# Kernel tuning notes

Measured on AMD Instinct MI355X. Metric: run time of the kernel, lower is better.

## Reference

```python
import jax, jax.numpy as jnp
import numpy as np

NUM_IMUS = 13
NUM_PARAMS = 9
EPS = 1e-5
LN_EPS = 1e-5


def setup_inputs() -> dict:
    key = jax.random.key(0)
    k1, k2, k3 = jax.random.split(key, 3)
    d_model, S = 512, 2048
    hidden_states = jax.random.normal(k1, (1, S, d_model), dtype=jnp.float32)
    min_orig_accel_norm = jax.random.normal(k2, (1,), dtype=jnp.float32)
    W = jax.random.normal(k3, (d_model, NUM_IMUS * NUM_PARAMS), dtype=jnp.float32) * 0.02
    b = jnp.zeros((NUM_IMUS * NUM_PARAMS,), jnp.float32)
    ln_w = jnp.ones((d_model,), jnp.float32)
    ln_b = jnp.zeros((d_model,), jnp.float32)
    return {"hidden_states": hidden_states, "min_orig_accel_norm": min_orig_accel_norm,
            "ln_w": ln_w, "ln_b": ln_b, "W": W, "b": b}


def _layernorm(x, w, bias):
    mu = x.mean(-1, keepdims=True)
    var = ((x - mu) ** 2).mean(-1, keepdims=True)
    return (x - mu) * jax.lax.rsqrt(var + LN_EPS) * w + bias


def reference(hidden_states, min_orig_accel_norm, ln_w, ln_b, W, b):
    S = hidden_states.shape[1]
    x = _layernorm(hidden_states, ln_w, ln_b)
    # (1,S,117) -> (S, 9, 13); batch is always 1
    p = (x @ W + b).reshape(S, NUM_PARAMS, NUM_IMUS)
    c, c_th, phi, phi_th = p[:, 4], p[:, 5], p[:, 6], p[:, 7]  # (S,13) each
    d = jnp.sqrt(p[:, 1] ** 2 + EPS)                 # (S,13)
    k = d ** 2 / 4 + jax.nn.softplus(p[:, 0])
    d_th = jnp.sqrt(p[:, 3] ** 2 + EPS)
    k_th = d_th ** 2 / 4 + jax.nn.softplus(p[:, 2])
    noise_bias = p[:, 8].T                           # (13,S)
    om = jnp.sqrt(4 * k - d ** 2) / 2                # = sqrt(softplus(p0))
    om_th = jnp.sqrt(4 * k_th - d_th ** 2) / 2
    t = jnp.arange(S, dtype=jnp.float32)
    tstep = jnp.triu(t[None, :] - t[:, None])        # (S,S), entry (i,j)=j-i for j>=i
    ts = tstep[:, :, None]                           # (S,S,1)

    def src(a):  # params indexed by source step i, broadcast over target step j
        return a[:, None, :]                         # (S,1,13)

    lin = src(c) * jnp.exp(-src(d) / 2 * ts) * jnp.sin(ts * src(om) + src(phi))
    ang = src(c_th) * jnp.exp(-src(d_th) / 2 * ts) * jnp.sin(ts * src(om_th) + src(phi_th))
    mask = jnp.triu(jnp.ones((S, S), jnp.float32))[:, :, None]
    summed = ((lin + ang) * mask).sum(axis=0)        # (S,13): sum over source i<=j
    return summed.T + min_orig_accel_norm + noise_bias  # (13,S)
```

## Files before the change

### kernel.cpp

```cpp
#include <hip/hip_runtime.h>
#include <math.h>

#define S_LEN 2048
#define D_MODEL 512
#define NIMU 13
#define NCOL 117
#define PCHUNK (S_LEN * NCOL)
#define WP_STRIDE 128

static __device__ __forceinline__ float softplus_f(float x) {
    return (x > 20.f) ? x : log1pf(expf(x));
}

__global__ __launch_bounds__(256) void stats_kernel(const float* __restrict__ H,
                                                    float2* __restrict__ stats,
                                                    const float* __restrict__ W,
                                                    float* __restrict__ Wp) {
    if (threadIdx.x < WP_STRIDE) {
        int c = threadIdx.x;
        Wp[blockIdx.x * WP_STRIDE + c] = (c < NCOL) ? W[blockIdx.x * NCOL + c] : 0.f;
    }
    int wave = threadIdx.x >> 6;
    int lane = threadIdx.x & 63;
    int row = blockIdx.x * 4 + wave;
    const float* hr = H + row * D_MODEL;
    float4 a = *(const float4*)&hr[lane * 4];
    float4 b = *(const float4*)&hr[256 + lane * 4];
    float sum = a.x + a.y + a.z + a.w + b.x + b.y + b.z + b.w;
    #pragma unroll
    for (int off = 32; off; off >>= 1) sum += __shfl_down(sum, off);
    sum = __shfl(sum, 0);
    float mu = sum * (1.f / 512.f);
    float vs = 0.f;
    vs += (a.x - mu) * (a.x - mu); vs += (a.y - mu) * (a.y - mu);
    vs += (a.z - mu) * (a.z - mu); vs += (a.w - mu) * (a.w - mu);
    vs += (b.x - mu) * (b.x - mu); vs += (b.y - mu) * (b.y - mu);
    vs += (b.z - mu) * (b.z - mu); vs += (b.w - mu) * (b.w - mu);
    #pragma unroll
    for (int off = 32; off; off >>= 1) vs += __shfl_down(vs, off);
    if (lane == 0) {
        float var = vs * (1.f / 512.f);
        stats[row] = make_float2(mu, 1.0f / sqrtf(var + 1e-5f));
    }
}

template <int ATOMIC>
__global__ __launch_bounds__(128) void proj_kernel(
    const float* __restrict__ H, const float2* __restrict__ stats,
    const float* __restrict__ lnw, const float* __restrict__ lnb,
    const float* __restrict__ Wp, float* __restrict__ Pout)
{
    __shared__ float Xt[64 * 32];
    __shared__ float Ws[64 * WP_STRIDE];
    int tid = threadIdx.x;
    int row0 = blockIdx.x * 32;
    int k0 = blockIdx.y * 64;

    {
        const float4* Wp4 = (const float4*)(Wp + k0 * WP_STRIDE);
        float4* Ws4 = (float4*)Ws;
        #pragma unroll
        for (int i = 0; i < 16; ++i) Ws4[tid + i * 128] = Wp4[tid + i * 128];
    }
    {
        int r = tid >> 2, fq = tid & 3;
        int row = row0 + r;
        float2 st = stats[row];
        const float4* H4 = (const float4*)(H + row * D_MODEL + k0);
        const float4* w4 = (const float4*)(lnw + k0);
        const float4* b4 = (const float4*)(lnb + k0);
        #pragma unroll
        for (int it = 0; it < 4; ++it) {
            int q = fq + it * 4;
            float4 h = H4[q], wv = w4[q], bv = b4[q];
            Xt[(4 * q + 0) * 32 + r] = (h.x - st.x) * st.y * wv.x + bv.x;
            Xt[(4 * q + 1) * 32 + r] = (h.y - st.x) * st.y * wv.y + bv.y;
            Xt[(4 * q + 2) * 32 + r] = (h.z - st.x) * st.y * wv.z + bv.z;
            Xt[(4 * q + 3) * 32 + r] = (h.w - st.x) * st.y * wv.w + bv.w;
        }
    }
    __syncthreads();

    int q8 = tid & 15;
    int rg = tid >> 4;
    float acc[4][8];
    #pragma unroll
    for (int a = 0; a < 4; ++a)
        for (int u = 0; u < 8; ++u) acc[a][u] = 0.f;

    #pragma unroll 4
    for (int k = 0; k < 64; ++k) {
        float4 xa = *(float4*)&Xt[k * 32 + 4 * rg];
        float4 w0 = *(float4*)&Ws[k * WP_STRIDE + 8 * q8];
        float4 w1 = *(float4*)&Ws[k * WP_STRIDE + 8 * q8 + 4];
        float xv[4] = {xa.x, xa.y, xa.z, xa.w};
        float wv[8] = {w0.x, w0.y, w0.z, w0.w, w1.x, w1.y, w1.z, w1.w};
        #pragma unroll
        for (int a = 0; a < 4; ++a)
            #pragma unroll
            for (int u = 0; u < 8; ++u)
                acc[a][u] = fmaf(xv[a], wv[u], acc[a][u]);
    }

    if (q8 < 15) {
        float* Pk = ATOMIC ? Pout : (Pout + blockIdx.y * PCHUNK);
        #pragma unroll
        for (int a = 0; a < 4; ++a) {
            int row = row0 + 4 * rg + a;
            #pragma unroll
            for (int u = 0; u < 8; ++u) {
                int c = 8 * q8 + u;
                if (c < NCOL) {
                    if (ATOMIC) atomicAdd(&Pk[row * NCOL + c], acc[a][u]);
                    else        Pk[row * NCOL + c] = acc[a][u];
                }
            }
        }
    }
}

__global__ __launch_bounds__(256) void transform_kernel(
    const float* __restrict__ Pp, int nkc,
    const float* __restrict__ bias, const float* __restrict__ minp,
    float4* __restrict__ PARL, float4* __restrict__ PARA,
    float* __restrict__ out)
{
    int t = blockIdx.x * 256 + threadIdx.x;
    if (t >= S_LEN * NIMU) return;
    int s = t / NIMU;
    int m = t - s * NIMU;
    float pv[9];
    #pragma unroll
    for (int pp = 0; pp < 9; ++pp) {
        float v = bias[pp * NIMU + m];
        for (int kc = 0; kc < nkc; ++kc)
            v += Pp[kc * PCHUNK + s * NCOL + pp * NIMU + m];
        pv[pp] = v;
    }

    const float LOG2E = 1.4426950408889634f;
    const float INV2PI = 0.15915494309189535f;
    {
        float d = sqrtf(pv[1] * pv[1] + 1e-5f);
        float kk = d * d * 0.25f + softplus_f(pv[0]);
        float om = 0.5f * sqrtf(fmaxf(4.f * kk - d * d, 0.f));
        PARL[m * S_LEN + s] = make_float4(pv[4], -0.5f * d * LOG2E, om * INV2PI, pv[6] * INV2PI);
    }
    {
        float d = sqrtf(pv[3] * pv[3] + 1e-5f);
        float kk = d * d * 0.25f + softplus_f(pv[2]);
        float om = 0.5f * sqrtf(fmaxf(4.f * kk - d * d, 0.f));
        PARA[m * S_LEN + s] = make_float4(pv[5], -0.5f * d * LOG2E, om * INV2PI, pv[7] * INV2PI);
    }
    out[m * S_LEN + s] = minp[0] + pv[8];
}

__global__ __launch_bounds__(256) void main_kernel(
    const float4* __restrict__ PARL, const float4* __restrict__ PARA,
    float* __restrict__ out)
{
    __shared__ float buf[4 * 192];
    int tid = threadIdx.x;
    int lane = tid & 63, w = tid >> 6;
    int m = blockIdx.y;
    int bx = blockIdx.x;

    int g = 0, base = 0;
    #pragma unroll 1
    for (;;) {
        int nb = ((g >> 1) + 4) >> 2;
        if (bx < base + nb) break;
        base += nb; ++g;
    }
    int sub = bx - base;
    int q = sub * 4 + w;
    int gsize = (g >> 1) + 1;

    float* accW = buf + w * 192;
    accW[lane] = 0.f; accW[lane + 64] = 0.f; accW[lane + 128] = 0.f;
    __builtin_amdgcn_wave_barrier();

    if (q < gsize) {
        int tc = q;
        int ic = g - 2 * q;
        int i = ic * 64 + lane;
        float4 pl = PARL[m * S_LEN + i];
        float4 pa = PARA[m * S_LEN + i];
        float ezL = __builtin_amdgcn_exp2f(pl.y);
        float zxL = ezL * __builtin_amdgcn_cosf(pl.z);
        float zyL = ezL * __builtin_amdgcn_sinf(pl.z);
        float ezA = __builtin_amdgcn_exp2f(pa.y);
        float zxA = ezA * __builtin_amdgcn_cosf(pa.z);
        float zyA = ezA * __builtin_amdgcn_sinf(pa.z);
        float dtf = (float)(tc * 128);
        float reL, imL, reA, imA;
        {
            float er = pl.x * __builtin_amdgcn_exp2f(dtf * pl.y);
            float r = fmaf(dtf, pl.z, pl.w); r -= floorf(r);
            reL = er * __builtin_amdgcn_cosf(r);
            imL = er * __builtin_amdgcn_sinf(r);
        }
        {
            float er = pa.x * __builtin_amdgcn_exp2f(dtf * pa.y);
            float r = fmaf(dtf, pa.z, pa.w); r -= floorf(r);
            reA = er * __builtin_amdgcn_cosf(r);
            imA = er * __builtin_amdgcn_sinf(r);
        }
        #pragma unroll 4
        for (int t = 0; t < 128; ++t) {
            accW[lane + t] += imL + imA;
            __builtin_amdgcn_wave_barrier();
            float nL = fmaf(reL, zxL, -(imL * zyL));
            imL = fmaf(reL, zyL, imL * zxL);
            reL = nL;
            float nA = fmaf(reA, zxA, -(imA * zyA));
            imA = fmaf(reA, zyA, imA * zxA);
            reA = nA;
        }
    }
    __syncthreads();
    if (tid < 192) {
        float s = buf[tid] + buf[192 + tid] + buf[384 + tid] + buf[576 + tid];
        int j = g * 64 + tid;
        if (j < S_LEN) atomicAdd(&out[m * S_LEN + j], s);
    }
}

extern "C" void kernel_launch(void* const* d_in, const int* in_sizes, int n_in,
                              void* d_out, int out_size, void* d_ws, size_t ws_size,
                              hipStream_t stream)
{
    const float* H    = (const float*)d_in[0];
    const float* MINP = (const float*)d_in[1];
    const float* LNW  = (const float*)d_in[2];
    const float* LNB  = (const float*)d_in[3];
    const float* W    = (const float*)d_in[4];
    const float* B    = (const float*)d_in[5];
    float* out = (float*)d_out;

    const size_t PSZ   = (size_t)PCHUNK * sizeof(float);
    const size_t STSZ  = S_LEN * sizeof(float2);
    const size_t PARSZ = (size_t)S_LEN * NIMU * sizeof(float4);
    const size_t need8 = 8 * PSZ + STSZ + 2 * PARSZ;

    char* ws = (char*)d_ws;
    if (ws_size >= need8) {
        float*  Pp    = (float*)ws;
        float2* stats = (float2*)(ws + 8 * PSZ);
        float4* PARL  = (float4*)(ws + 8 * PSZ + STSZ);
        float4* PARA  = (float4*)(ws + 8 * PSZ + STSZ + PARSZ);
        float*  Wp    = (float*)PARL;
        stats_kernel<<<512, 256, 0, stream>>>(H, stats, W, Wp);
        proj_kernel<0><<<dim3(64, 8), 128, 0, stream>>>(H, stats, LNW, LNB, Wp, Pp);
        transform_kernel<<<(S_LEN * NIMU + 255) / 256, 256, 0, stream>>>(Pp, 8, B, MINP, PARL, PARA, out);
        main_kernel<<<dim3(80, NIMU), 256, 0, stream>>>(PARL, PARA, out);
    } else {
        float*  P     = (float*)ws;
        float2* stats = (float2*)(ws + PSZ);
        float4* PARL  = (float4*)(ws + PSZ + STSZ);
        float4* PARA  = (float4*)(ws + PSZ + STSZ + PARSZ);
        float*  Wp    = (float*)PARL;
        hipMemsetAsync(P, 0, PSZ, stream);
        stats_kernel<<<512, 256, 0, stream>>>(H, stats, W, Wp);
        proj_kernel<1><<<dim3(64, 8), 128, 0, stream>>>(H, stats, LNW, LNB, Wp, P);
        transform_kernel<<<(S_LEN * NIMU + 255) / 256, 256, 0, stream>>>(P, 1, B, MINP, PARL, PARA, out);
        main_kernel<<<dim3(80, NIMU), 256, 0, stream>>>(PARL, PARA, out);
    }
}
```

Baseline: 112.2 us.

## Fuse parameter transform into main kernel with transposed partials and 128-step tiles

Removes the separate transform kernel. The projection now writes transposed, column-major partial sums so the main kernel can read them coalesced, reduce the split-K chunks, and compute the oscillator parameters itself. The main kernel's tiles grow to 128 source rows, with two oscillator sets per lane, which halves the number of blocks. Output zeroing moves into the stats kernel, and the noise bias is added by the first block of each diagonal group. This cuts one launch and the intermediate PARL/PARA round-trip, but each main block now redoes the split-K reduction and transcendental setup, and the atomic-fallback path is dropped.

```diff
diff --git a/kernel.cpp b/kernel.cpp
--- a/kernel.cpp
+++ b/kernel.cpp
@@ -5,20 +5,43 @@
 #define D_MODEL 512
 #define NIMU 13
 #define NCOL 117
-#define PCHUNK (S_LEN * NCOL)
-#define WP_STRIDE 128
+#define CPAD 128
+#define NKC 8
+#define KCSTRIDE ((size_t)CPAD * S_LEN)
 
 static __device__ __forceinline__ float softplus_f(float x) {
     return (x > 20.f) ? x : log1pf(expf(x));
+}
+
+static __device__ __forceinline__ void osc_init(float pk, float pd, float amp, float phi, float dtf,
+                                                float& re, float& im, float& zr, float& zi)
+{
+    const float LOG2E = 1.4426950408889634f;
+    const float INV2PI = 0.15915494309189535f;
+    float d = sqrtf(pd * pd + 1e-5f);
+    float kk = d * d * 0.25f + softplus_f(pk);
+    float om = 0.5f * sqrtf(fmaxf(4.f * kk - d * d, 0.f));
+    float y = -0.5f * d * LOG2E;
+    float f = om * INV2PI;
+    float ph = phi * INV2PI;
+    float ez = __builtin_amdgcn_exp2f(y);
+    zr = ez * __builtin_amdgcn_cosf(f);
+    zi = ez * __builtin_amdgcn_sinf(f);
+    float er = amp * __builtin_amdgcn_exp2f(dtf * y);
+    float r = fmaf(dtf, f, ph); r -= floorf(r);
+    re = er * __builtin_amdgcn_cosf(r);
+    im = er * __builtin_amdgcn_sinf(r);
 }
 
 __global__ __launch_bounds__(256) void stats_kernel(const float* __restrict__ H,
                                                     float2* __restrict__ stats,
                                                     const float* __restrict__ W,
-                                                    float* __restrict__ Wp) {
-    if (threadIdx.x < WP_STRIDE) {
+                                                    float* __restrict__ Wp,
+                                                    float* __restrict__ out) {
+    if (blockIdx.x < 104) out[blockIdx.x * 256 + threadIdx.x] = 0.f;
+    if (threadIdx.x < CPAD) {
         int c = threadIdx.x;
-        Wp[blockIdx.x * WP_STRIDE + c] = (c < NCOL) ? W[blockIdx.x * NCOL + c] : 0.f;
+        Wp[blockIdx.x * CPAD + c] = (c < NCOL) ? W[blockIdx.x * NCOL + c] : 0.f;
     }
     int wave = threadIdx.x >> 6;
     int lane = threadIdx.x & 63;
@@ -44,20 +67,19 @@
     }
 }
 
-template <int ATOMIC>
 __global__ __launch_bounds__(128) void proj_kernel(
     const float* __restrict__ H, const float2* __restrict__ stats,
     const float* __restrict__ lnw, const float* __restrict__ lnb,
-    const float* __restrict__ Wp, float* __restrict__ Pout)
+    const float* __restrict__ Wp, float* __restrict__ Pt)
 {
     __shared__ float Xt[64 * 32];
-    __shared__ float Ws[64 * WP_STRIDE];
+    __shared__ float Ws[64 * CPAD];
     int tid = threadIdx.x;
     int row0 = blockIdx.x * 32;
     int k0 = blockIdx.y * 64;
 
     {
-        const float4* Wp4 = (const float4*)(Wp + k0 * WP_STRIDE);
+        const float4* Wp4 = (const float4*)(Wp + k0 * CPAD);
         float4* Ws4 = (float4*)Ws;
         #pragma unroll
         for (int i = 0; i < 16; ++i) Ws4[tid + i * 128] = Wp4[tid + i * 128];
@@ -91,8 +113,8 @@
     #pragma unroll 4
     for (int k = 0; k < 64; ++k) {
         float4 xa = *(float4*)&Xt[k * 32 + 4 * rg];
-        float4 w0 = *(float4*)&Ws[k * WP_STRIDE + 8 * q8];
-        float4 w1 = *(float4*)&Ws[k * WP_STRIDE + 8 * q8 + 4];
+        float4 w0 = *(float4*)&Ws[k * CPAD + 8 * q8];
+        float4 w1 = *(float4*)&Ws[k * CPAD + 8 * q8 + 4];
         float xv[4] = {xa.x, xa.y, xa.z, xa.w};
         float wv[8] = {w0.x, w0.y, w0.z, w0.w, w1.x, w1.y, w1.z, w1.w};
         #pragma unroll
@@ -103,63 +125,22 @@
     }
 
     if (q8 < 15) {
-        float* Pk = ATOMIC ? Pout : (Pout + blockIdx.y * PCHUNK);
-        #pragma unroll
-        for (int a = 0; a < 4; ++a) {
-            int row = row0 + 4 * rg + a;
-            #pragma unroll
-            for (int u = 0; u < 8; ++u) {
-                int c = 8 * q8 + u;
-                if (c < NCOL) {
-                    if (ATOMIC) atomicAdd(&Pk[row * NCOL + c], acc[a][u]);
-                    else        Pk[row * NCOL + c] = acc[a][u];
-                }
+        #pragma unroll
+        for (int u = 0; u < 8; ++u) {
+            int c = 8 * q8 + u;
+            if (c < NCOL) {
+                float4 v = make_float4(acc[0][u], acc[1][u], acc[2][u], acc[3][u]);
+                *(float4*)&Pt[((size_t)blockIdx.y * CPAD + c) * S_LEN + row0 + 4 * rg] = v;
             }
         }
     }
 }
 
-__global__ __launch_bounds__(256) void transform_kernel(
-    const float* __restrict__ Pp, int nkc,
-    const float* __restrict__ bias, const float* __restrict__ minp,
-    float4* __restrict__ PARL, float4* __restrict__ PARA,
-    float* __restrict__ out)
-{
-    int t = blockIdx.x * 256 + threadIdx.x;
-    if (t >= S_LEN * NIMU) return;
-    int s = t / NIMU;
-    int m = t - s * NIMU;
-    float pv[9];
-    #pragma unroll
-    for (int pp = 0; pp < 9; ++pp) {
-        float v = bias[pp * NIMU + m];
-        for (int kc = 0; kc < nkc; ++kc)
-            v += Pp[kc * PCHUNK + s * NCOL + pp * NIMU + m];
-        pv[pp] = v;
-    }
-
-    const float LOG2E = 1.4426950408889634f;
-    const float INV2PI = 0.15915494309189535f;
-    {
-        float d = sqrtf(pv[1] * pv[1] + 1e-5f);
-        float kk = d * d * 0.25f + softplus_f(pv[0]);
-        float om = 0.5f * sqrtf(fmaxf(4.f * kk - d * d, 0.f));
-        PARL[m * S_LEN + s] = make_float4(pv[4], -0.5f * d * LOG2E, om * INV2PI, pv[6] * INV2PI);
-    }
-    {
-        float d = sqrtf(pv[3] * pv[3] + 1e-5f);
-        float kk = d * d * 0.25f + softplus_f(pv[2]);
-        float om = 0.5f * sqrtf(fmaxf(4.f * kk - d * d, 0.f));
-        PARA[m * S_LEN + s] = make_float4(pv[5], -0.5f * d * LOG2E, om * INV2PI, pv[7] * INV2PI);
-    }
-    out[m * S_LEN + s] = minp[0] + pv[8];
-}
-
 __global__ __launch_bounds__(256) void main_kernel(
-    const float4* __restrict__ PARL, const float4* __restrict__ PARA,
-    float* __restrict__ out)
-{
-    __shared__ float buf[4 * 192];
+    const float* __restrict__ Pt, const float* __restrict__ bias,
+    const float* __restrict__ minp, float* __restrict__ out)
+{
+    __shared__ float buf[4 * 256];
     int tid = threadIdx.x;
     int lane = tid & 63, w = tid >> 6;
     int m = blockIdx.y;
@@ -168,61 +149,77 @@
     int g = 0, base = 0;
     #pragma unroll 1
     for (;;) {
-        int nb = ((g >> 1) + 4) >> 2;
+        int nb = (g + 4) >> 2;
         if (bx < base + nb) break;
         base += nb; ++g;
     }
     int sub = bx - base;
     int q = sub * 4 + w;
-    int gsize = (g >> 1) + 1;
-
-    float* accW = buf + w * 192;
-    accW[lane] = 0.f; accW[lane + 64] = 0.f; accW[lane + 128] = 0.f;
+
+    float* accW = buf + w * 256;
+    accW[lane] = 0.f; accW[lane + 64] = 0.f;
+    accW[lane + 128] = 0.f; accW[lane + 192] = 0.f;
     __builtin_amdgcn_wave_barrier();
 
-    if (q < gsize) {
-        int tc = q;
-        int ic = g - 2 * q;
-        int i = ic * 64 + lane;
-        float4 pl = PARL[m * S_LEN + i];
-        float4 pa = PARA[m * S_LEN + i];
-        float ezL = __builtin_amdgcn_exp2f(pl.y);
-        float zxL = ezL * __builtin_amdgcn_cosf(pl.z);
-        float zyL = ezL * __builtin_amdgcn_sinf(pl.z);
-        float ezA = __builtin_amdgcn_exp2f(pa.y);
-        float zxA = ezA * __builtin_amdgcn_cosf(pa.z);
-        float zyA = ezA * __builtin_amdgcn_sinf(pa.z);
+    if (q <= g) {
+        int sc = q, tc = g - q;
+        int i0 = sc * 128;
         float dtf = (float)(tc * 128);
-        float reL, imL, reA, imA;
-        {
-            float er = pl.x * __builtin_amdgcn_exp2f(dtf * pl.y);
-            float r = fmaf(dtf, pl.z, pl.w); r -= floorf(r);
-            reL = er * __builtin_amdgcn_cosf(r);
-            imL = er * __builtin_amdgcn_sinf(r);
-        }
-        {
-            float er = pa.x * __builtin_amdgcn_exp2f(dtf * pa.y);
-            float r = fmaf(dtf, pa.z, pa.w); r -= floorf(r);
-            reA = er * __builtin_amdgcn_cosf(r);
-            imA = er * __builtin_amdgcn_sinf(r);
-        }
-        #pragma unroll 4
+
+        float pvA[9], pvB[9];
+        #pragma unroll
+        for (int p = 0; p < 9; ++p) {
+            int c = p * 13 + m;
+            const float* bp = Pt + (size_t)c * S_LEN + i0 + lane;
+            float vA = bias[c], vB = vA;
+            #pragma unroll
+            for (int kc = 0; kc < NKC; ++kc) {
+                vA += bp[kc * KCSTRIDE];
+                vB += bp[kc * KCSTRIDE + 64];
+            }
+            pvA[p] = vA; pvB[p] = vB;
+        }
+
+        float reLA, imLA, zrLA, ziLA; osc_init(pvA[0], pvA[1], pvA[4], pvA[6], dtf, reLA, imLA, zrLA, ziLA);
+        float reAA, imAA, zrAA, ziAA; osc_init(pvA[2], pvA[3], pvA[5], pvA[7], dtf, reAA, imAA, zrAA, ziAA);
+        float reLB, imLB, zrLB, ziLB; osc_init(pvB[0], pvB[1], pvB[4], pvB[6], dtf, reLB, imLB, zrLB, ziLB);
+        float reAB, imAB, zrAB, ziAB; osc_init(pvB[2], pvB[3], pvB[5], pvB[7], dtf, reAB, imAB, zrAB, ziAB);
+
+        #pragma unroll 8
         for (int t = 0; t < 128; ++t) {
-            accW[lane + t] += imL + imA;
+            float a0 = accW[lane + t];
+            float a1 = accW[lane + 64 + t];
+            a0 += imLA + imAA;
+            a1 += imLB + imAB;
+            accW[lane + t] = a0;
+            accW[lane + 64 + t] = a1;
             __builtin_amdgcn_wave_barrier();
-            float nL = fmaf(reL, zxL, -(imL * zyL));
-            imL = fmaf(reL, zyL, imL * zxL);
-            reL = nL;
-            float nA = fmaf(reA, zxA, -(imA * zyA));
-            imA = fmaf(reA, zyA, imA * zxA);
-            reA = nA;
+            float tL = imLA * ziLA; float rL = fmaf(reLA, zrLA, -tL);
+            imLA = fmaf(reLA, ziLA, imLA * zrLA); reLA = rL;
+            float tA = imAA * ziAA; float rA = fmaf(reAA, zrAA, -tA);
+            imAA = fmaf(reAA, ziAA, imAA * zrAA); reAA = rA;
+            float tLB = imLB * ziLB; float rLB = fmaf(reLB, zrLB, -tLB);
+            imLB = fmaf(reLB, ziLB, imLB * zrLB); reLB = rLB;
+            float tAB = imAB * ziAB; float rAB = fmaf(reAB, zrAB, -tAB);
+            imAB = fmaf(reAB, ziAB, imAB * zrAB); reAB = rAB;
         }
     }
     __syncthreads();
-    if (tid < 192) {
-        float s = buf[tid] + buf[192 + tid] + buf[384 + tid] + buf[576 + tid];
-        int j = g * 64 + tid;
-        if (j < S_LEN) atomicAdd(&out[m * S_LEN + j], s);
+
+    {
+        int j = g * 128 + tid;
+        if (j < S_LEN) {
+            float s = buf[tid] + buf[256 + tid] + buf[512 + tid] + buf[768 + tid];
+            if (sub == 0 && tid < 128) {
+                int c8 = 8 * 13 + m;
+                float v = minp[0] + bias[c8];
+                const float* bp = Pt + (size_t)c8 * S_LEN + j;
+                #pragma unroll
+                for (int kc = 0; kc < NKC; ++kc) v += bp[kc * KCSTRIDE];
+                s += v;
+            }
+            atomicAdd(&out[m * S_LEN + j], s);
+        }
     }
 }
 
@@ -238,32 +235,15 @@
     const float* B    = (const float*)d_in[5];
     float* out = (float*)d_out;
 
-    const size_t PSZ   = (size_t)PCHUNK * sizeof(float);
-    const size_t STSZ  = S_LEN * sizeof(float2);
-    const size_t PARSZ = (size_t)S_LEN * NIMU * sizeof(float4);
-    const size_t need8 = 8 * PSZ + STSZ + 2 * PARSZ;
+    const size_t PTSZ = (size_t)NKC * CPAD * S_LEN * sizeof(float);
+    const size_t STSZ = S_LEN * sizeof(float2);
 
     char* ws = (char*)d_ws;
-    if (ws_size >= need8) {
-        float*  Pp    = (float*)ws;
-        float2* stats = (float2*)(ws + 8 * PSZ);
-        float4* PARL  = (float4*)(ws + 8 * PSZ + STSZ);
-        float4* PARA  = (float4*)(ws + 8 * PSZ + STSZ + PARSZ);
-        float*  Wp    = (float*)PARL;
-        stats_kernel<<<512, 256, 0, stream>>>(H, stats, W, Wp);
-        proj_kernel<0><<<dim3(64, 8), 128, 0, stream>>>(H, stats, LNW, LNB, Wp, Pp);
-        transform_kernel<<<(S_LEN * NIMU + 255) / 256, 256, 0, stream>>>(Pp, 8, B, MINP, PARL, PARA, out);
-        main_kernel<<<dim3(80, NIMU), 256, 0, stream>>>(PARL, PARA, out);
-    } else {
-        float*  P     = (float*)ws;
-        float2* stats = (float2*)(ws + PSZ);
-        float4* PARL  = (float4*)(ws + PSZ + STSZ);
-        float4* PARA  = (float4*)(ws + PSZ + STSZ + PARSZ);
-        float*  Wp    = (float*)PARL;
-        hipMemsetAsync(P, 0, PSZ, stream);
-        stats_kernel<<<512, 256, 0, stream>>>(H, stats, W, Wp);
-        proj_kernel<1><<<dim3(64, 8), 128, 0, stream>>>(H, stats, LNW, LNB, Wp, P);
-        transform_kernel<<<(S_LEN * NIMU + 255) / 256, 256, 0, stream>>>(P, 1, B, MINP, PARL, PARA, out);
-        main_kernel<<<dim3(80, NIMU), 256, 0, stream>>>(PARL, PARA, out);
-    }
-}
+    float*  Pt    = (float*)ws;
+    float2* stats = (float2*)(ws + PTSZ);
+    float*  Wp    = (float*)(ws + PTSZ + STSZ);
+
+    stats_kernel<<<512, 256, 0, stream>>>(H, stats, W, Wp, out);
+    proj_kernel<<<dim3(64, 8), 128, 0, stream>>>(H, stats, LNW, LNB, Wp, Pt);
+    main_kernel<<<dim3(40, NIMU), 256, 0, stream>>>(Pt, B, MINP, out);
+}
```

Result: faster. 98.33 us, median of 2 (-12.3%).
